# Kernel tuning notes

Measured on AMD Instinct MI355X. Metric: run time of the kernel, lower is better.

The kernel has to match this reference:

```python
import jax, jax.numpy as jnp
import numpy as np

B, S, H, D = 8, 4096, 1024, 256  # batch, seq, hidden_size, state_size


def setup_inputs() -> dict:
    key = jax.random.key(0)
    ks = jax.random.split(key, 4)
    scale_in = 1.0 / np.sqrt(H)
    scale_st = 1.0 / np.sqrt(D)
    return {
        "x": jax.random.normal(ks[0], (B, S, H), dtype=jnp.float32),
        "W_in": jax.random.normal(ks[1], (H, D), dtype=jnp.float32) * scale_in,
        "b_in": jnp.zeros((D,), dtype=jnp.float32),
        "W_state": jax.random.normal(ks[2], (D, D), dtype=jnp.float32) * scale_st,
        "b_state": jnp.zeros((D,), dtype=jnp.float32),
        "W_out": jax.random.normal(ks[3], (D, H), dtype=jnp.float32) * scale_st,
        "b_out": jnp.zeros((H,), dtype=jnp.float32),
    }


def reference(x, W_in, b_in, W_state, b_state, W_out, b_out):
    # Precompute input projection for all timesteps in one big GEMM: [B,S,D]
    inp = jnp.einsum("bsh,hd->bsd", x, W_in) + b_in

    def step(state, inp_t):
        # state: [B,D], inp_t: [B,D]
        state = jnp.tanh(inp_t + state @ W_state + b_state)
        return state, state

    state0 = jnp.zeros((x.shape[0], W_state.shape[0]), dtype=x.dtype)
    # scan over time axis -> states: [S,B,D]
    _, states = jax.lax.scan(step, state0, jnp.swapaxes(inp, 0, 1))
    # output projection: [S,B,H] -> [B,S,H]
    out = jnp.einsum("sbd,dh->sbh", states, W_out) + b_out
    return jnp.swapaxes(out, 0, 1)
```

## Files before the change

kernel.cpp:

```cpp
#include <hip/hip_runtime.h>
#include <stdint.h>


typedef float v4f __attribute__((ext_vector_type(4)));
typedef __bf16 bf16x4 __attribute__((ext_vector_type(4)));
typedef __bf16 bf16x8 __attribute__((ext_vector_type(8)));
typedef _Float16 h8 __attribute__((ext_vector_type(8)));

#define BARRIER_LGKM() asm volatile("s_waitcnt lgkmcnt(0)\n\ts_barrier" ::: "memory")

#define GLOAD_LDS16(g, l)                                                    \
  __builtin_amdgcn_global_load_lds(                                          \
      (const __attribute__((address_space(1))) void*)(g),                    \
      (__attribute__((address_space(3))) void*)(l), 16, 0, 0)

#define GETREG_HWID  __builtin_amdgcn_s_getreg(0xF804)
#define GETREG_XCCID __builtin_amdgcn_s_getreg(0xF814)

#define AT_LOAD(p)     __hip_atomic_load((p), __ATOMIC_RELAXED, __HIP_MEMORY_SCOPE_AGENT)
#define AT_STORE(p, v) __hip_atomic_store((p), (v), __ATOMIC_RELAXED, __HIP_MEMORY_SCOPE_AGENT)
#define AT_ADD(p, v)   __hip_atomic_fetch_add((p), (v), __ATOMIC_RELAXED, __HIP_MEMORY_SCOPE_AGENT)
#define FENCE_ACQ() __builtin_amdgcn_fence(__ATOMIC_ACQUIRE, "agent")
#define FENCE_REL() __builtin_amdgcn_fence(__ATOMIC_RELEASE, "agent")

#define CTL_NEXT 0
#define CTL_REG  1
#define CTL_PROG 2
#define CTL_SCU  10
#define CTL_EXIT 18
#define CTL_G1   32

__global__ void cvt_f32_bf16_x4(const float* __restrict__ in,
                                __bf16* __restrict__ out, int n4) {
  int i = blockIdx.x * blockDim.x + threadIdx.x;
  if (i >= n4) return;
  v4f v = ((const v4f*)in)[i];
  bf16x4 o;
  o.x = (__bf16)v.x; o.y = (__bf16)v.y; o.z = (__bf16)v.z; o.w = (__bf16)v.w;
  ((bf16x4*)out)[i] = o;
}

__global__ void transpose_cvt(const float* __restrict__ in,
                              __bf16* __restrict__ out, int K, int N) {
  int i = blockIdx.x * blockDim.x + threadIdx.x;
  if (i >= K * N) return;
  int k = i / N;
  int n = i - k * N;
  out[(size_t)n * K + k] = (__bf16)in[i];
}

__global__ void zero_ctl(uint32_t* p) { p[threadIdx.x] = 0; }

__device__ __forceinline__ void gemm128(
    const __bf16* __restrict__ A, const __bf16* __restrict__ Bt,
    const float* __restrict__ bias, float* __restrict__ C,
    int N, int K, int m0, int n0, char* lds, int tid) {
  const int lane = tid & 63;
  const int w = tid >> 6;
  const int wr = w >> 1, wc = w & 1;
  const int r = lane & 15, q = lane >> 4;

  const __bf16* gA[2];
  const __bf16* gB[2];
  int loff[2];
#pragma unroll
  for (int j = 0; j < 2; ++j) {
    int o = (w * 2 + j) * 1024 + lane * 16;
    int row = o >> 6;
    int s = (o >> 4) & 3;
    int ss = s ^ ((row >> 1) & 3);
    gA[j] = A + (size_t)(m0 + row) * K + ss * 8;
    gB[j] = Bt + (size_t)(n0 + row) * K + ss * 8;
    loff[j] = (w * 2 + j) * 1024;
  }

  const int slot = (q ^ ((r >> 1) & 3)) * 16;
  int aoff[4], boff[4];
#pragma unroll
  for (int i = 0; i < 4; ++i) {
    aoff[i] = (wr * 64 + i * 16 + r) * 64 + slot;
    boff[i] = 8192 + (wc * 64 + i * 16 + r) * 64 + slot;
  }

  v4f acc[4][4];
#pragma unroll
  for (int mi = 0; mi < 4; ++mi)
#pragma unroll
    for (int ni = 0; ni < 4; ++ni) acc[mi][ni] = (v4f){0.f, 0.f, 0.f, 0.f};

  const int NK = K >> 5;
#pragma unroll
  for (int j = 0; j < 2; ++j) {
    GLOAD_LDS16(gA[j], lds + loff[j]);
    GLOAD_LDS16(gB[j], lds + 8192 + loff[j]);
  }

  for (int kt = 0; kt < NK; ++kt) {
    __syncthreads();
    if (kt + 1 < NK) {
      char* lb = lds + ((kt + 1) & 1) * 16384;
      const int ke = (kt + 1) * 32;
#pragma unroll
      for (int j = 0; j < 2; ++j) {
        GLOAD_LDS16(gA[j] + ke, lb + loff[j]);
        GLOAD_LDS16(gB[j] + ke, lb + 8192 + loff[j]);
      }
    }
    const char* Lb = lds + (kt & 1) * 16384;
    bf16x8 af[4], bf[4];
#pragma unroll
    for (int i = 0; i < 4; ++i) af[i] = *(const bf16x8*)(Lb + aoff[i]);
#pragma unroll
    for (int i = 0; i < 4; ++i) bf[i] = *(const bf16x8*)(Lb + boff[i]);
#pragma unroll
    for (int mi = 0; mi < 4; ++mi)
#pragma unroll
      for (int ni = 0; ni < 4; ++ni)
        acc[mi][ni] = __builtin_amdgcn_mfma_f32_16x16x32_bf16(
            af[mi], bf[ni], acc[mi][ni], 0, 0, 0);
  }

  float bv[4];
#pragma unroll
  for (int ni = 0; ni < 4; ++ni) bv[ni] = bias[n0 + wc * 64 + ni * 16 + r];
#pragma unroll
  for (int mi = 0; mi < 4; ++mi) {
    int rowb = m0 + wr * 64 + mi * 16 + q * 4;
#pragma unroll
    for (int ni = 0; ni < 4; ++ni) {
      int col = n0 + wc * 64 + ni * 16 + r;
      float* cp = C + (size_t)rowb * N + col;
#pragma unroll
      for (int i = 0; i < 4; ++i) cp[(size_t)i * N] = acc[mi][ni][i] + bv[ni];
    }
  }
}

__global__ __launch_bounds__(512) void fused(
    const __bf16* __restrict__ xb,
    const __bf16* __restrict__ WinT,
    const float* __restrict__ b_in,
    float* __restrict__ inp,
    const float* __restrict__ Wst,
    const float* __restrict__ b_state,
    __bf16* __restrict__ states,
    const __bf16* __restrict__ WoutT,
    const float* __restrict__ b_out,
    float* __restrict__ out,
    uint32_t* __restrict__ ctl, int S) {
  const int tid = threadIdx.x;
  __shared__ __align__(16) char ldsAll[65552];

  uint32_t* progress = ctl + CTL_PROG;
  uint32_t* scanCU = ctl + CTL_SCU;
  uint32_t* g1flag = ctl + CTL_G1;

  if (blockIdx.x < 8) {
    const int b = blockIdx.x;
    const int l = tid & 63;
    const int q = l >> 4;
    const int r = l & 15;
    const int w = tid >> 6;

    if (tid == 0) {
      uint32_t id = ((GETREG_HWID >> 8) & 0xFF) | (GETREG_XCCID << 8);
      AT_STORE(&scanCU[b], id);
      __hip_atomic_fetch_add(&ctl[CTL_REG], 1u, __ATOMIC_RELEASE,
                             __HIP_MEMORY_SCOPE_AGENT);
    }

    h8 bwA[8], bwB[8];
#pragma unroll
    for (int c = 0; c < 8; ++c) {
#pragma unroll
      for (int i = 0; i < 8; ++i) {
        const float* wp = Wst + (size_t)(32 * c + 8 * q + i) * 256 + 32 * w + r;
        bwA[c][i] = (_Float16)wp[0];
        bwB[c][i] = (_Float16)wp[16];
      }
    }

    const int col = 32 * w + 16 * (q & 1) + r;
    const float bst = b_state[col];
    const float* inpb = inp + (size_t)b * S * 256;
    __bf16* stb = states + (size_t)b * S * 256;

    if (tid == 0) {
      while (AT_LOAD(&g1flag[b]) == 0) __builtin_amdgcn_s_sleep(8);
    }
    __syncthreads();
    FENCE_ACQ();

    _Float16* sbuf = (_Float16*)ldsAll;
    if (tid < 256) sbuf[tid] = (_Float16)0.f;
    float u_cur = inpb[col];
    float u_nxt = inpb[256 + col];
    __syncthreads();

    int cur = 0;
    for (int t = 0; t < S; ++t) {
      if ((t + 2 < S) && (((t + 2) & 127) == 0)) {
        const int c = (t + 2) >> 7;
        if (tid == 0) {
          while (AT_LOAD(&g1flag[c * 8 + b]) == 0) __builtin_amdgcn_s_sleep(8);
        }
        __syncthreads();
        FENCE_ACQ();
      }
      float u_n2 = 0.f;
      if (t + 2 < S) u_n2 = inpb[(size_t)(t + 2) * 256 + col];

      const h8* sp = (const h8*)(ldsAll + cur * 512);
      h8 af[8];
#pragma unroll
      for (int c = 0; c < 8; ++c) af[c] = sp[4 * c + q];

      v4f a0 = {0.f, 0.f, 0.f, 0.f};
      v4f a1 = a0;
#pragma unroll
      for (int c = 0; c < 8; ++c) {
        a0 = __builtin_amdgcn_mfma_f32_16x16x32_f16(af[c], bwA[c], a0, 0, 0, 0);
        a1 = __builtin_amdgcn_mfma_f32_16x16x32_f16(af[c], bwB[c], a1, 0, 0, 0);
      }
      float x = ((q & 1) ? a1[0] : a0[0]) + u_cur + bst;

      float e = exp2f(2.885390082f * x);
      float sn = 1.f - 2.f * __builtin_amdgcn_rcpf(e + 1.f);

      cur ^= 1;
      if (q < 2) {
        ((_Float16*)ldsAll)[cur * 256 + col] = (_Float16)sn;
        stb[(size_t)t * 256 + col] = (__bf16)sn;
      }
      if ((t & 127) == 127) {
        asm volatile("s_waitcnt vmcnt(0)" ::: "memory");
        __syncthreads();
        if (tid == 0) {
          FENCE_REL();
          AT_STORE(&progress[b], (uint32_t)(t + 1));
        }
      }
      u_cur = u_nxt;
      u_nxt = u_n2;
      BARRIER_LGKM();
    }
  } else {
    volatile uint32_t* bc = (volatile uint32_t*)(ldsAll + 65536);
    if (tid == 0) {
      while (__hip_atomic_load(&ctl[CTL_REG], __ATOMIC_ACQUIRE,
                               __HIP_MEMORY_SCOPE_AGENT) < 8)
        __builtin_amdgcn_s_sleep(8);
      uint32_t id = ((GETREG_HWID >> 8) & 0xFF) | (GETREG_XCCID << 8);
      uint32_t clash = 0;
#pragma unroll
      for (int i = 0; i < 8; ++i)
        if (AT_LOAD(&scanCU[i]) == id) clash = 1;
      uint32_t doexit = 0;
      if (clash && AT_ADD(&ctl[CTL_EXIT], 1u) < 16) doexit = 1;
      *bc = doexit;
    }
    __syncthreads();
    if (*bc) return;

    const int sub = tid >> 8;
    const int stid = tid & 255;
    char* myl = ldsAll + sub * 32768;

    for (;;) {
      __syncthreads();
      if (tid == 0) *bc = AT_ADD(&ctl[CTL_NEXT], 1u);
      __syncthreads();
      uint32_t P = *bc;
      if (P >= 1280) return;

      if (P < 256) {
        const int c = P >> 3, b = P & 7;
        const int m0 = b * 4096 + c * 128;
        gemm128(xb, WinT, b_in, inp, 256, 1024, m0, sub * 128, myl, stid);
        asm volatile("s_waitcnt vmcnt(0)" ::: "memory");
        __syncthreads();
        if (tid == 0) {
          FENCE_REL();
          AT_STORE(&g1flag[P], 1u);
        }
      } else {
        const uint32_t Q = P - 256;
        const int mc = Q >> 5, b = (Q >> 2) & 7, np = Q & 3;
        if (tid == 0) {
          const uint32_t need = (uint32_t)(mc + 1) * 128;
          while (AT_LOAD(&progress[b]) < need) __builtin_amdgcn_s_sleep(64);
        }
        __syncthreads();
        FENCE_ACQ();
        const int m0 = b * 4096 + mc * 128;
        gemm128(states, WoutT, b_out, out, 1024, 256, m0,
                (np * 2 + sub) * 128, myl, stid);
      }
    }
  }
}

extern "C" void kernel_launch(void* const* d_in, const int* in_sizes, int n_in,
                              void* d_out, int out_size, void* d_ws,
                              size_t ws_size, hipStream_t stream) {
  const float* x       = (const float*)d_in[0];
  const float* W_in    = (const float*)d_in[1];
  const float* b_in    = (const float*)d_in[2];
  const float* W_state = (const float*)d_in[3];
  const float* b_state = (const float*)d_in[4];
  const float* W_out   = (const float*)d_in[5];
  const float* b_out   = (const float*)d_in[6];
  float* out = (float*)d_out;

  const int B = 8, S = 4096, H = 1024, D = 256;
  const int M = B * S;

  char* ws = (char*)d_ws;
  float*  inp    = (float*)(ws + 0);
  __bf16* states = (__bf16*)(ws + 33554432);
  __bf16* xb     = (__bf16*)(ws + 50331648);
  __bf16* WinT   = (__bf16*)(ws + 117440512);
  __bf16* WoutT  = (__bf16*)(ws + 117964800);
  uint32_t* ctl  = (uint32_t*)(ws + 118489088);

  cvt_f32_bf16_x4<<<(M * H / 4 + 255) / 256, 256, 0, stream>>>(x, xb, M * H / 4);
  transpose_cvt<<<(H * D + 255) / 256, 256, 0, stream>>>(W_in, WinT, H, D);
  transpose_cvt<<<(D * H + 255) / 256, 256, 0, stream>>>(W_out, WoutT, D, H);
  zero_ctl<<<1, 512, 0, stream>>>(ctl);

  fused<<<248, 512, 0, stream>>>(xb, WinT, b_in, inp, W_state, b_state,
                                 states, WoutT, b_out, out, ctl, S);
}
```

Baseline: 2.293 ms.

## Fuse fp32-to-bf16 input conversion into GEMM and shrink worker grid

```diff
diff --git a/kernel.cpp b/kernel.cpp
--- a/kernel.cpp
+++ b/kernel.cpp
@@ -3,7 +3,6 @@
 
 
 typedef float v4f __attribute__((ext_vector_type(4)));
-typedef __bf16 bf16x4 __attribute__((ext_vector_type(4)));
 typedef __bf16 bf16x8 __attribute__((ext_vector_type(8)));
 typedef _Float16 h8 __attribute__((ext_vector_type(8)));
 
@@ -30,33 +29,32 @@
 #define CTL_EXIT 18
 #define CTL_G1   32
 
-__global__ void cvt_f32_bf16_x4(const float* __restrict__ in,
-                                __bf16* __restrict__ out, int n4) {
+#define NWORK 64
+#define NPAIR 1280
+
+__global__ void transpose_cvt2(const float* __restrict__ W_in,
+                               __bf16* __restrict__ WinT,
+                               const float* __restrict__ W_out,
+                               __bf16* __restrict__ WoutT) {
   int i = blockIdx.x * blockDim.x + threadIdx.x;
-  if (i >= n4) return;
-  v4f v = ((const v4f*)in)[i];
-  bf16x4 o;
-  o.x = (__bf16)v.x; o.y = (__bf16)v.y; o.z = (__bf16)v.z; o.w = (__bf16)v.w;
-  ((bf16x4*)out)[i] = o;
+  if (i < 1024 * 256) {
+    int k = i >> 8, n = i & 255;
+    WinT[(size_t)n * 1024 + k] = (__bf16)W_in[i];
+  } else {
+    int j = i - 1024 * 256;
+    int k = j >> 10, n = j & 1023;
+    WoutT[(size_t)n * 256 + k] = (__bf16)W_out[j];
+  }
 }
 
-__global__ void transpose_cvt(const float* __restrict__ in,
-                              __bf16* __restrict__ out, int K, int N) {
-  int i = blockIdx.x * blockDim.x + threadIdx.x;
-  if (i >= K * N) return;
-  int k = i / N;
-  int n = i - k * N;
-  out[(size_t)n * K + k] = (__bf16)in[i];
-}
-
 __global__ void zero_ctl(uint32_t* p) { p[threadIdx.x] = 0; }
 
-__device__ __forceinline__ void gemm128(
+__device__ __forceinline__ void gemm_bt_body(
     const __bf16* __restrict__ A, const __bf16* __restrict__ Bt,
     const float* __restrict__ bias, float* __restrict__ C,
-    int N, int K, int m0, int n0, char* lds, int tid) {
-  const int lane = tid & 63;
-  const int w = tid >> 6;
+    int N, int K, int m0, int n0, char* lds, int stid) {
+  const int lane = stid & 63;
+  const int w = stid >> 6;
   const int wr = w >> 1, wc = w & 1;
   const int r = lane & 15, q = lane >> 4;
 
@@ -73,7 +71,6 @@
     gB[j] = Bt + (size_t)(n0 + row) * K + ss * 8;
     loff[j] = (w * 2 + j) * 1024;
   }
-
   const int slot = (q ^ ((r >> 1) & 3)) * 16;
   int aoff[4], boff[4];
 #pragma unroll
@@ -81,7 +78,6 @@
     aoff[i] = (wr * 64 + i * 16 + r) * 64 + slot;
     boff[i] = 8192 + (wc * 64 + i * 16 + r) * 64 + slot;
   }
-
   v4f acc[4][4];
 #pragma unroll
   for (int mi = 0; mi < 4; ++mi)
@@ -94,7 +90,6 @@
     GLOAD_LDS16(gA[j], lds + loff[j]);
     GLOAD_LDS16(gB[j], lds + 8192 + loff[j]);
   }
-
   for (int kt = 0; kt < NK; ++kt) {
     __syncthreads();
     if (kt + 1 < NK) {
@@ -119,7 +114,6 @@
         acc[mi][ni] = __builtin_amdgcn_mfma_f32_16x16x32_bf16(
             af[mi], bf[ni], acc[mi][ni], 0, 0, 0);
   }
-
   float bv[4];
 #pragma unroll
   for (int ni = 0; ni < 4; ++ni) bv[ni] = bias[n0 + wc * 64 + ni * 16 + r];
@@ -136,8 +130,127 @@
   }
 }
 
+__device__ __forceinline__ void gemm_xf_body(
+    const float* __restrict__ A, const __bf16* __restrict__ Bt,
+    const float* __restrict__ bias, float* __restrict__ C,
+    int N, int K, int m0, int n0, char* lds, int stid) {
+  const int lane = stid & 63;
+  const int w = stid >> 6;
+  const int wr = w >> 1, wc = w & 1;
+  const int r = lane & 15, q = lane >> 4;
+
+  const int arow = stid >> 1;
+  const int h = stid & 1;
+  const int sw = (arow >> 1) & 3;
+  const int g0 = (2 * h) ^ sw;
+  const int g1 = (2 * h + 1) ^ sw;
+  const float* gAsrc = A + (size_t)(m0 + arow) * K;
+  const int awoff = arow * 64 + 2 * h * 16;
+
+  const __bf16* gB[2];
+  int loffB[2];
+#pragma unroll
+  for (int j = 0; j < 2; ++j) {
+    int o = (w * 2 + j) * 1024 + lane * 16;
+    int row = o >> 6;
+    int s = (o >> 4) & 3;
+    int ss = s ^ ((row >> 1) & 3);
+    gB[j] = Bt + (size_t)(n0 + row) * K + ss * 8;
+    loffB[j] = 8192 + (w * 2 + j) * 1024;
+  }
+  const int slot = (q ^ ((r >> 1) & 3)) * 16;
+  int aoff[4], boff[4];
+#pragma unroll
+  for (int i = 0; i < 4; ++i) {
+    aoff[i] = (wr * 64 + i * 16 + r) * 64 + slot;
+    boff[i] = 8192 + (wc * 64 + i * 16 + r) * 64 + slot;
+  }
+  v4f acc[4][4];
+#pragma unroll
+  for (int mi = 0; mi < 4; ++mi)
+#pragma unroll
+    for (int ni = 0; ni < 4; ++ni) acc[mi][ni] = (v4f){0.f, 0.f, 0.f, 0.f};
+
+  const int NK = K >> 5;
+  {
+    v4f a0 = *(const v4f*)(gAsrc + g0 * 8);
+    v4f a1 = *(const v4f*)(gAsrc + g0 * 8 + 4);
+    v4f a2 = *(const v4f*)(gAsrc + g1 * 8);
+    v4f a3 = *(const v4f*)(gAsrc + g1 * 8 + 4);
+#pragma unroll
+    for (int j = 0; j < 2; ++j) GLOAD_LDS16(gB[j], lds + loffB[j]);
+    bf16x8 w0, w1;
+#pragma unroll
+    for (int i = 0; i < 4; ++i) {
+      w0[i] = (__bf16)a0[i]; w0[4 + i] = (__bf16)a1[i];
+      w1[i] = (__bf16)a2[i]; w1[4 + i] = (__bf16)a3[i];
+    }
+    *(bf16x8*)(lds + awoff) = w0;
+    *(bf16x8*)(lds + awoff + 16) = w1;
+  }
+  for (int kt = 0; kt < NK; ++kt) {
+    __syncthreads();
+    const int nxt = kt + 1;
+    v4f a0, a1, a2, a3;
+    if (nxt < NK) {
+      const float* s = gAsrc + nxt * 32;
+      a0 = *(const v4f*)(s + g0 * 8);
+      a1 = *(const v4f*)(s + g0 * 8 + 4);
+      a2 = *(const v4f*)(s + g1 * 8);
+      a3 = *(const v4f*)(s + g1 * 8 + 4);
+#pragma unroll
+      for (int j = 0; j < 2; ++j)
+        GLOAD_LDS16(gB[j] + nxt * 32, lds + (nxt & 1) * 16384 + loffB[j] - 0 +
+                                          0),
+            (void)0;
+    }
+    if (nxt < NK) {
+#pragma unroll
+      for (int j = 0; j < 2; ++j)
+        GLOAD_LDS16(gB[j] + nxt * 32, lds + (nxt & 1) * 16384 + loffB[j]);
+    }
+    const char* Lb = lds + (kt & 1) * 16384;
+    bf16x8 af[4], bf[4];
+#pragma unroll
+    for (int i = 0; i < 4; ++i) af[i] = *(const bf16x8*)(Lb + aoff[i]);
+#pragma unroll
+    for (int i = 0; i < 4; ++i) bf[i] = *(const bf16x8*)(Lb + boff[i]);
+#pragma unroll
+    for (int mi = 0; mi < 4; ++mi)
+#pragma unroll
+      for (int ni = 0; ni < 4; ++ni)
+        acc[mi][ni] = __builtin_amdgcn_mfma_f32_16x16x32_bf16(
+            af[mi], bf[ni], acc[mi][ni], 0, 0, 0);
+    if (nxt < NK) {
+      bf16x8 w0, w1;
+#pragma unroll
+      for (int i = 0; i < 4; ++i) {
+        w0[i] = (__bf16)a0[i]; w0[4 + i] = (__bf16)a1[i];
+        w1[i] = (__bf16)a2[i]; w1[4 + i] = (__bf16)a3[i];
+      }
+      char* Ln = lds + (nxt & 1) * 16384;
+      *(bf16x8*)(Ln + awoff) = w0;
+      *(bf16x8*)(Ln + awoff + 16) = w1;
+    }
+  }
+  float bv[4];
+#pragma unroll
+  for (int ni = 0; ni < 4; ++ni) bv[ni] = bias[n0 + wc * 64 + ni * 16 + r];
+#pragma unroll
+  for (int mi = 0; mi < 4; ++mi) {
+    int rowb = m0 + wr * 64 + mi * 16 + q * 4;
+#pragma unroll
+    for (int ni = 0; ni < 4; ++ni) {
+      int col = n0 + wc * 64 + ni * 16 + r;
+      float* cp = C + (size_t)rowb * N + col;
+#pragma unroll
+      for (int i = 0; i < 4; ++i) cp[(size_t)i * N] = acc[mi][ni][i] + bv[ni];
+    }
+  }
+}
+
 __global__ __launch_bounds__(512) void fused(
-    const __bf16* __restrict__ xb,
+    const float* __restrict__ x,
     const __bf16* __restrict__ WinT,
     const float* __restrict__ b_in,
     float* __restrict__ inp,
@@ -193,22 +306,24 @@
 
     _Float16* sbuf = (_Float16*)ldsAll;
     if (tid < 256) sbuf[tid] = (_Float16)0.f;
-    float u_cur = inpb[col];
-    float u_nxt = inpb[256 + col];
+    float u0 = inpb[col];
+    float u1 = inpb[256 + col];
+    float u2 = inpb[512 + col];
+    float u3 = inpb[768 + col];
     __syncthreads();
 
     int cur = 0;
     for (int t = 0; t < S; ++t) {
-      if ((t + 2 < S) && (((t + 2) & 127) == 0)) {
-        const int c = (t + 2) >> 7;
+      if ((t + 4 < S) && (((t + 4) & 127) == 0)) {
+        const int c = (t + 4) >> 7;
         if (tid == 0) {
           while (AT_LOAD(&g1flag[c * 8 + b]) == 0) __builtin_amdgcn_s_sleep(8);
         }
         __syncthreads();
         FENCE_ACQ();
       }
-      float u_n2 = 0.f;
-      if (t + 2 < S) u_n2 = inpb[(size_t)(t + 2) * 256 + col];
+      float un = 0.f;
+      if (t + 4 < S) un = inpb[(size_t)(t + 4) * 256 + col];
 
       const h8* sp = (const h8*)(ldsAll + cur * 512);
       h8 af[8];
@@ -222,9 +337,9 @@
         a0 = __builtin_amdgcn_mfma_f32_16x16x32_f16(af[c], bwA[c], a0, 0, 0, 0);
         a1 = __builtin_amdgcn_mfma_f32_16x16x32_f16(af[c], bwB[c], a1, 0, 0, 0);
       }
-      float x = ((q & 1) ? a1[0] : a0[0]) + u_cur + bst;
-
-      float e = exp2f(2.885390082f * x);
+      float xv = ((q & 1) ? a1[0] : a0[0]) + u0 + bst;
+
+      float e = exp2f(2.885390082f * xv);
       float sn = 1.f - 2.f * __builtin_amdgcn_rcpf(e + 1.f);
 
       cur ^= 1;
@@ -232,17 +347,18 @@
         ((_Float16*)ldsAll)[cur * 256 + col] = (_Float16)sn;
         stb[(size_t)t * 256 + col] = (__bf16)sn;
       }
-      if ((t & 127) == 127) {
-        asm volatile("s_waitcnt vmcnt(0)" ::: "memory");
-        __syncthreads();
-        if (tid == 0) {
-          FENCE_REL();
-          AT_STORE(&progress[b], (uint32_t)(t + 1));
-        }
-      }
-      u_cur = u_nxt;
-      u_nxt = u_n2;
+      if ((t & 127) == 32 && t >= 160 && tid == 0) {
+        FENCE_REL();
+        AT_STORE(&progress[b], (uint32_t)(t - 32));
+      }
+      u0 = u1; u1 = u2; u2 = u3; u3 = un;
       BARRIER_LGKM();
+    }
+    asm volatile("s_waitcnt vmcnt(0)" ::: "memory");
+    __syncthreads();
+    if (tid == 0) {
+      FENCE_REL();
+      AT_STORE(&progress[b], (uint32_t)S);
     }
   } else {
     volatile uint32_t* bc = (volatile uint32_t*)(ldsAll + 65536);
@@ -271,12 +387,12 @@
       if (tid == 0) *bc = AT_ADD(&ctl[CTL_NEXT], 1u);
       __syncthreads();
       uint32_t P = *bc;
-      if (P >= 1280) return;
+      if (P >= NPAIR) return;
 
       if (P < 256) {
         const int c = P >> 3, b = P & 7;
         const int m0 = b * 4096 + c * 128;
-        gemm128(xb, WinT, b_in, inp, 256, 1024, m0, sub * 128, myl, stid);
+        gemm_xf_body(x, WinT, b_in, inp, 256, 1024, m0, sub * 128, myl, stid);
         asm volatile("s_waitcnt vmcnt(0)" ::: "memory");
         __syncthreads();
         if (tid == 0) {
@@ -293,8 +409,8 @@
         __syncthreads();
         FENCE_ACQ();
         const int m0 = b * 4096 + mc * 128;
-        gemm128(states, WoutT, b_out, out, 1024, 256, m0,
-                (np * 2 + sub) * 128, myl, stid);
+        gemm_bt_body(states, WoutT, b_out, out, 1024, 256, m0,
+                     (np * 2 + sub) * 128, myl, stid);
       }
     }
   }
@@ -312,22 +428,18 @@
   const float* b_out   = (const float*)d_in[6];
   float* out = (float*)d_out;
 
-  const int B = 8, S = 4096, H = 1024, D = 256;
-  const int M = B * S;
+  const int B = 8, S = 4096;
 
   char* ws = (char*)d_ws;
   float*  inp    = (float*)(ws + 0);
   __bf16* states = (__bf16*)(ws + 33554432);
-  __bf16* xb     = (__bf16*)(ws + 50331648);
-  __bf16* WinT   = (__bf16*)(ws + 117440512);
-  __bf16* WoutT  = (__bf16*)(ws + 117964800);
-  uint32_t* ctl  = (uint32_t*)(ws + 118489088);
-
-  cvt_f32_bf16_x4<<<(M * H / 4 + 255) / 256, 256, 0, stream>>>(x, xb, M * H / 4);
-  transpose_cvt<<<(H * D + 255) / 256, 256, 0, stream>>>(W_in, WinT, H, D);
-  transpose_cvt<<<(D * H + 255) / 256, 256, 0, stream>>>(W_out, WoutT, D, H);
+  __bf16* WinT   = (__bf16*)(ws + 50331648);
+  __bf16* WoutT  = (__bf16*)(ws + 50855936);
+  uint32_t* ctl  = (uint32_t*)(ws + 51380224);
+
+  transpose_cvt2<<<2048, 256, 0, stream>>>(W_in, WinT, W_out, WoutT);
   zero_ctl<<<1, 512, 0, stream>>>(ctl);
 
-  fused<<<248, 512, 0, stream>>>(xb, WinT, b_in, inp, W_state, b_state,
-                                 states, WoutT, b_out, out, ctl, S);
+  fused<<<8 + NWORK, 512, 0, stream>>>(x, WinT, b_in, inp, W_state, b_state,
+                                       states, WoutT, b_out, out, ctl, S);
 }
```

Result: slower. 2.353 ms (+2.6%).
